# Optimization experiments

Hardware: AMD Instinct MI355X
Metric: run time of the kernel (lower is better)

## Reference

```python
import jax, jax.numpy as jnp
import numpy as np
from jax import lax

B, F_, C, H, W = 2, 1, 128, 48, 160
D = 96
MIN_DEPTH, MAX_DEPTH = 0.1, 20.0


def setup_inputs() -> dict:
    key = jax.random.key(0)
    k1, k2, k3, k4 = jax.random.split(key, 4)
    current_feats = jax.random.normal(k1, (B, C, H, W), dtype=jnp.float32)
    lookup_feats = jax.random.normal(k2, (B, F_, C, H, W), dtype=jnp.float32)
    # relative poses: identity rotation + small random translation (nonzero sum -> frame is used)
    t = np.asarray(jax.random.normal(k3, (B, F_, 3))) * 0.1
    poses = np.tile(np.eye(4, dtype=np.float32), (B, F_, 1, 1))
    poses[:, :, :3, 3] = t
    # KITTI-like intrinsics scaled to the 48x160 matching resolution
    Km = np.eye(4, dtype=np.float32)
    Km[0, 0] = 0.58 * W
    Km[1, 1] = 1.92 * H
    Km[0, 2] = 0.5 * W
    Km[1, 2] = 0.5 * H
    K = np.tile(Km, (B, 1, 1))
    invK = np.tile(np.linalg.inv(Km), (B, 1, 1))
    conv_w = jax.random.normal(k4, (C, C + D, 3, 3), dtype=jnp.float32) * 0.02
    conv_b = jnp.zeros((C,), dtype=jnp.float32)
    return {
        'current_feats': current_feats,
        'lookup_feats': lookup_feats,
        'poses': jnp.asarray(poses),
        'K': jnp.asarray(K),
        'invK': jnp.asarray(invK),
        'conv_w': conv_w,
        'conv_b': conv_b,
    }


def _plane_sweep(current_feats, lookup_feats, poses, K, invK):
    depth_bins = jnp.linspace(MIN_DEPTH, MAX_DEPTH, D).astype(jnp.float32)
    # homogeneous pixel grid [3, HW] (x, y, 1), matching BackprojectDepth
    xs, ys = jnp.meshgrid(jnp.arange(W, dtype=jnp.float32), jnp.arange(H, dtype=jnp.float32), indexing='xy')
    pix = jnp.stack([xs.ravel(), ys.ravel(), jnp.ones(H * W, jnp.float32)], 0)  # [3, HW]
    # backproject: world points per batch and depth plane -> [B, D, 4, HW]
    cam = jnp.einsum('bij,jn->bin', invK[:, :3, :3], pix)                        # [B, 3, HW]
    world = depth_bins[None, :, None, None] * cam[:, None]                       # [B, D, 3, HW]
    ones = jnp.ones((B, D, 1, H * W), jnp.float32)
    world4 = jnp.concatenate([world, ones], axis=2)                              # [B, D, 4, HW]
    # project into lookup frames (Project3D): P = (K @ T)[:3]
    P = jnp.einsum('bij,bfjk->bfik', K, poses)[:, :, :3, :]                      # [B, F, 3, 4]
    campts = jnp.einsum('bfij,bdjn->bfdin', P, world4)                           # [B, F, D, 3, HW]
    xy = campts[:, :, :, :2] / (campts[:, :, :, 2:3] + 1e-7)                     # [B, F, D, 2, HW]
    gx = xy[:, :, :, 0].reshape(B, F_, D, H, W)  # pixel x coords (align_corners=True round-trip is exact)
    gy = xy[:, :, :, 1].reshape(B, F_, D, H, W)
    # bilinear grid_sample with zeros padding
    x0 = jnp.floor(gx)
    y0 = jnp.floor(gy)
    wx = gx - x0
    wy = gy - y0
    x0i = x0.astype(jnp.int32)
    y0i = y0.astype(jnp.int32)
    x1i = x0i + 1
    y1i = y0i + 1
    feat_flat = lookup_feats.reshape(B, F_, C, H * W)
    warped = jnp.zeros((B, F_, D, C, H * W), jnp.float32)
    for xi, yi, w in ((x0i, y0i, (1 - wx) * (1 - wy)), (x1i, y0i, wx * (1 - wy)),
                      (x0i, y1i, (1 - wx) * wy), (x1i, y1i, wx * wy)):
        valid = (xi >= 0) & (xi < W) & (yi >= 0) & (yi < H)
        idx = (jnp.clip(yi, 0, H - 1) * W + jnp.clip(xi, 0, W - 1)).reshape(B, F_, D, H * W)
        vals = jnp.take_along_axis(feat_flat[:, :, None], idx[:, :, :, None], axis=4)  # [B,F,D,C,HW]
        warped = warped + vals * (w * valid.astype(jnp.float32)).reshape(B, F_, D, 1, H * W)
    warped = warped.reshape(B, F_, D, C, H, W)
    # edge mask (valid reprojections away from borders)
    edge = ((gx >= 2.0) & (gx <= W - 2) & (gy >= 2.0) & (gy <= H - 2)).astype(jnp.float32)
    interior = jnp.zeros((H, W), jnp.float32).at[2:-2, 2:-2].set(1.0)
    edge = edge * interior  # [B, F, D, H, W]
    # skip frames whose pose sums to zero
    vp = (jnp.sum(poses, axis=(2, 3)) != 0).astype(jnp.float32)                  # [B, F]
    diffs = jnp.abs(warped - current_feats[:, None, None]).mean(axis=3)          # [B, F, D, H, W]
    diffs = diffs * edge * vp[:, :, None, None, None]
    cost = jnp.sum(diffs, axis=1)                                                # [B, D, H, W]
    counts = jnp.sum((diffs > 0).astype(jnp.float32), axis=1)
    cost = cost / (counts + 1e-7)
    missing = (cost == 0).astype(jnp.float32)
    cost = cost * (1 - missing) + jnp.max(cost, axis=1, keepdims=True) * missing
    conf = (jnp.sum((cost * (1 - missing)) > 0, axis=1) == D).astype(jnp.float32)  # [B, H, W]
    viz = jnp.where(cost == 0, 100.0, cost)
    argmin = jnp.argmin(viz, axis=1)                                             # [B, H, W]
    lowest_cost = 1.0 / depth_bins[argmin]
    return cost, conf, lowest_cost


def reference(current_feats, lookup_feats, poses, K, invK, conv_w, conv_b):
    cost, conf, lowest_cost = _plane_sweep(current_feats, lookup_feats, poses, K, invK)
    cost = cost * conf[:, None]
    cat = jnp.concatenate([current_feats, cost], axis=1)                         # [B, C+D, H, W]
    out = lax.conv_general_dilated(cat, conv_w, (1, 1), 'SAME',
                                   dimension_numbers=('NCHW', 'OIHW', 'NCHW'))
    out = jax.nn.relu(out + conv_b[None, :, None, None])
    return out, lowest_cost, conf
```

## Files before the change

kernel.cpp:

```cpp
#include <hip/hip_runtime.h>
#include <hip/hip_bf16.h>

#define BB 2
#define CC 128
#define HH 48
#define WW 160
#define DD 96
#define HWp (HH*WW)
#define CIN 224
#define NKC 63
#define H2 50
#define W2 162
#define PSTR 392

typedef __bf16 bf16_t;
typedef __bf16 bf16x8 __attribute__((ext_vector_type(8)));
typedef float  f32x4  __attribute__((ext_vector_type(4)));
typedef float  f32x2  __attribute__((ext_vector_type(2)));

union ABFrag { uint4 u; bf16x8 v; };
union PackW  { bf16_t h[8]; uint4 u; };
union F4     { float4 f; f32x2 h[2]; };
union PK4    { bf16_t h[4]; uint2 u; };

#define CATP_U4 453600

__global__ __launch_bounds__(256) void k_prep(
    const float* __restrict__ look, const float* __restrict__ cw,
    float* __restrict__ lookT, bf16_t* __restrict__ wPack,
    bf16_t* __restrict__ catP) {
  int z = blockIdx.y;
  if (z < 2) {
    __shared__ float tile[CC * 65];
    int bIdx = z;
    const float* src = look + (size_t)bIdx * CC * HWp;
    int p0 = blockIdx.x * 64;
    int tid = threadIdx.x;
    int px = tid & 63, cb = tid >> 6;
    #pragma unroll
    for (int k = 0; k < 32; k++) {
      int c = k * 4 + cb;
      tile[c * 65 + px] = src[(size_t)c * HWp + p0 + px];
    }
    __syncthreads();
    int ci = tid & 127, pb = tid >> 7;
    #pragma unroll
    for (int k = 0; k < 32; k++) {
      int pp = k * 2 + pb;
      lookT[((size_t)bIdx * HWp + p0 + pp) * CC + ci] = tile[ci * 65 + pp];
    }
  } else if (z == 2) {
    for (int t = blockIdx.x * 256 + threadIdx.x; t < 8 * NKC * 64; t += 120 * 256) {
      int lane = t & 63;
      int kc = (t >> 6) % NKC;
      int nt = t / (NKC * 64);
      int co = nt * 16 + (lane & 15);
      int kbase = kc * 32 + (lane >> 4) * 8;
      PackW tmp;
      #pragma unroll
      for (int j = 0; j < 8; j++) {
        int kk = kbase + j;
        int tap = kk / 224, ci2 = kk % 224;
        int ky = tap / 3, kx = tap % 3;
        tmp.h[j] = (bf16_t)cw[(((size_t)co * 224 + ci2) * 3 + ky) * 3 + kx];
      }
      *(uint4*)(wPack + (size_t)t * 8) = tmp.u;
    }
  } else {
    uint4 zz = make_uint4(0u, 0u, 0u, 0u);
    uint4* cp = (uint4*)catP;
    for (int t = blockIdx.x * 256 + threadIdx.x; t < CATP_U4; t += 120 * 256)
      cp[t] = zz;
  }
}

__global__ __launch_bounds__(256) void k_cost(
    const float* __restrict__ cur, const float* __restrict__ lookT,
    const float* __restrict__ poses, const float* __restrict__ Kmat,
    const float* __restrict__ invK,
    bf16_t* __restrict__ catP, float* __restrict__ outLow,
    float* __restrict__ outConf) {
  __shared__ float partialL[8 * PSTR];
  __shared__ __align__(4) bf16_t fillL[8 * 96];

  int tid = threadIdx.x;
  int b = blockIdx.y;
  int wv = tid >> 6;
  int lane = tid & 63;
  int pix = lane >> 3;
  int l = lane & 7;
  int p = blockIdx.x * 8 + pix;
  int hh = p / WW, ww = p % WW;

  const float* Kb  = Kmat + b * 16;
  const float* Tb  = poses + b * 16;
  const float* iKb = invK + b * 16;
  float P[3][4];
  #pragma unroll
  for (int i = 0; i < 3; i++)
    #pragma unroll
    for (int j = 0; j < 4; j++)
      P[i][j] = Kb[i*4+0]*Tb[0*4+j] + Kb[i*4+1]*Tb[1*4+j]
              + Kb[i*4+2]*Tb[2*4+j] + Kb[i*4+3]*Tb[3*4+j];
  float psum = 0.0f;
  #pragma unroll
  for (int i = 0; i < 16; i++) psum += Tb[i];
  bool vpnz = (psum != 0.0f);

  float x = (float)ww, y = (float)hh;
  float cam0 = iKb[0]*x + iKb[1]*y + iKb[2];
  float cam1 = iKb[4]*x + iKb[5]*y + iKb[6];
  float cam2 = iKb[8]*x + iKb[9]*y + iKb[10];
  float qx = P[0][0]*cam0 + P[0][1]*cam1 + P[0][2]*cam2;
  float qy = P[1][0]*cam0 + P[1][1]*cam1 + P[1][2]*cam2;
  float qz = P[2][0]*cam0 + P[2][1]*cam1 + P[2][2]*cam2;
  float px3 = P[0][3], py3 = P[1][3], pz3 = P[2][3];
  bool interior = (hh >= 2 && hh <= HH-3 && ww >= 2 && ww <= WW-3);
  bool groupValid = interior && vpnz;

  int l4 = l * 4;
  F4 negCur[4];
  #pragma unroll
  for (int s4 = 0; s4 < 4; s4++) {
    float4 t;
    t.x = cur[((size_t)(b * CC + l4 + s4 * 32 + 0)) * HWp + p];
    t.y = cur[((size_t)(b * CC + l4 + s4 * 32 + 1)) * HWp + p];
    t.z = cur[((size_t)(b * CC + l4 + s4 * 32 + 2)) * HWp + p];
    t.w = cur[((size_t)(b * CC + l4 + s4 * 32 + 3)) * HWp + p];
    F4 tt; tt.f = t;
    negCur[s4].h[0] = -tt.h[0];
    negCur[s4].h[1] = -tt.h[1];
  }
  bf16_t* pixBase = catP + (((size_t)b * H2 + hh + 1) * W2 + (ww + 1)) * CIN;
  if (wv == 0) {
    #pragma unroll
    for (int s4 = 0; s4 < 4; s4++) {
      PK4 pk;
      pk.h[0] = (bf16_t)(-negCur[s4].f.x);
      pk.h[1] = (bf16_t)(-negCur[s4].f.y);
      pk.h[2] = (bf16_t)(-negCur[s4].f.z);
      pk.h[3] = (bf16_t)(-negCur[s4].f.w);
      *(uint2*)(pixBase + l4 + s4 * 32) = pk.u;
    }
  }

  const float* lookB = lookT + (size_t)b * HWp * CC;
  const float stepd = (20.0f - 0.1f) / 95.0f;

  int prevCell = -1;
  float x0f = 0.0f, y0f = 0.0f;
  F4 v00[4], v10[4], v01[4], v11[4];
  #pragma unroll
  for (int s4 = 0; s4 < 4; s4++) {
    v00[s4].f = make_float4(0.f,0.f,0.f,0.f);
    v10[s4].f = make_float4(0.f,0.f,0.f,0.f);
    v01[s4].f = make_float4(0.f,0.f,0.f,0.f);
    v11[s4].f = make_float4(0.f,0.f,0.f,0.f);
  }

  for (int dd = 0; dd < 24; dd++) {
    int d = wv * 24 + dd;
    float depth = 0.1f + (float)d * stepd;
    float s = 0.0f;
    if (groupValid) {
      float cxx = fmaf(depth, qx, px3);
      float cyy = fmaf(depth, qy, py3);
      float czz = fmaf(depth, qz, pz3);
      float r = __builtin_amdgcn_rcpf(czz + 1e-7f);
      float gx = cxx * r, gy = cyy * r;
      if (gx >= 2.0f && gx <= (float)(WW-2) && gy >= 2.0f && gy <= (float)(HH-2)) {
        float xf = floorf(gx), yf = floorf(gy);
        int x0 = (int)xf, y0 = (int)yf;
        int cell = y0 * WW + x0;
        if (cell != prevCell) {
          prevCell = cell; x0f = xf; y0f = yf;
          const float* bp0 = lookB + ((size_t)cell * CC + l4);
          const float* bp1 = bp0 + WW * CC;
          #pragma unroll
          for (int s4 = 0; s4 < 4; s4++) {
            v00[s4].f = *(const float4*)(bp0 + s4 * 32);
            v10[s4].f = *(const float4*)(bp0 + s4 * 32 + CC);
            v01[s4].f = *(const float4*)(bp1 + s4 * 32);
            v11[s4].f = *(const float4*)(bp1 + s4 * 32 + CC);
          }
        }
        float wx = gx - x0f, wy = gy - y0f;
        float w11v = wx * wy;
        float w10v = wx - w11v, w01v = wy - w11v;
        float w00v = 1.0f - wx - wy + w11v;
        f32x2 W00 = {w00v, w00v}, W10 = {w10v, w10v};
        f32x2 W01 = {w01v, w01v}, W11 = {w11v, w11v};
        f32x2 accA = {0.f, 0.f}, accB = {0.f, 0.f};
        #pragma unroll
        for (int s4 = 0; s4 < 4; s4++) {
          #pragma unroll
          for (int hf = 0; hf < 2; hf++) {
            f32x2 t = negCur[s4].h[hf];
            t = __builtin_elementwise_fma(W00, v00[s4].h[hf], t);
            t = __builtin_elementwise_fma(W10, v10[s4].h[hf], t);
            t = __builtin_elementwise_fma(W01, v01[s4].h[hf], t);
            t = __builtin_elementwise_fma(W11, v11[s4].h[hf], t);
            f32x2 a = __builtin_elementwise_max(t, -t);
            if (s4 & 1) accB += a; else accA += a;
          }
        }
        f32x2 accT = accA + accB;
        s = accT.x + accT.y;
      }
    }
    s += __shfl_xor(s, 1, 8);
    if ((l & 1) == 0) partialL[pix * PSTR + d * 4 + (l >> 1)] = s;
  }
  __syncthreads();

  const float kScale = 1.0f / 128.0f / (1.0f + 1e-7f);
  int pix2 = tid >> 5, g = tid & 31;
  int p2 = blockIdx.x * 8 + pix2;
  int hh2 = p2 / WW, ww2 = p2 % WW;
  float c3[3];
  float m0 = 0.0f;
  int ct = 0;
  #pragma unroll
  for (int k = 0; k < 3; k++) {
    int d = g + 32 * k;
    const float4 pp = *(const float4*)&partialL[pix2 * PSTR + d * 4];
    float c = ((pp.x + pp.y) + (pp.z + pp.w)) * kScale;
    c3[k] = c;
    m0 = fmaxf(m0, c);
    ct += (c > 0.0f) ? 1 : 0;
  }
  #pragma unroll
  for (int off = 1; off < 32; off <<= 1) {
    m0 = fmaxf(m0, __shfl_xor(m0, off, 32));
    ct += __shfl_xor(ct, off, 32);
  }
  float confF = (ct == DD) ? 1.0f : 0.0f;
  float minv = 3.4e38f;
  int mind = 0x7fffffff;
  #pragma unroll
  for (int k = 0; k < 3; k++) {
    int d = g + 32 * k;
    float c = c3[k];
    float filled = (c == 0.0f) ? m0 : c;
    float viz = (filled == 0.0f) ? 100.0f : filled;
    if (viz < minv) { minv = viz; mind = d; }
    fillL[pix2 * 96 + d] = (bf16_t)(filled * confF);
  }
  #pragma unroll
  for (int off = 1; off < 32; off <<= 1) {
    float ov = __shfl_xor(minv, off, 32);
    int   oi = __shfl_xor(mind, off, 32);
    if (ov < minv || (ov == minv && oi < mind)) { minv = ov; mind = oi; }
  }
  if (g == 0) {
    outLow[(size_t)b * HWp + p2] = 1.0f / (0.1f + (float)mind * (20.0f - 0.1f) / 95.0f);
    outConf[(size_t)b * HWp + p2] = confF;
  }
  __syncthreads();
  const unsigned* fu = (const unsigned*)fillL;
  unsigned* cu = (unsigned*)(catP + (((size_t)b * H2 + hh2 + 1) * W2 + (ww2 + 1)) * CIN + CC);
  #pragma unroll
  for (int k = 0; k < 2; k++) {
    int idx = g + 32 * k;
    if (idx < 48) cu[idx] = fu[pix2 * 48 + idx];
  }
}

__global__ __launch_bounds__(256) void k_conv(
    const bf16_t* __restrict__ catP, const bf16_t* __restrict__ wPack,
    const float* __restrict__ bias, float* __restrict__ out) {
  int wave = threadIdx.x >> 6;
  int lane = threadIdx.x & 63;
  int m16 = lane & 15, quad = lane >> 4;
  int tile = blockIdx.x * 4 + wave;
  int nt0 = blockIdx.y * 2;
  int P0 = tile * 16;
  int b = P0 / HWp;
  int rp = P0 % HWp;
  int h = rp / WW, w0 = rp % WW;

  f32x4 acc[2];
  #pragma unroll
  for (int j = 0; j < 2; j++) { f32x4 z = {0.f,0.f,0.f,0.f}; acc[j] = z; }

  #pragma unroll
  for (int tap = 0; tap < 9; tap++) {
    int dy = tap / 3 - 1, dx = tap % 3 - 1;
    const bf16_t* ap = catP
      + ((size_t)(b * H2 + h + dy + 1) * W2 + (w0 + m16 + dx + 1)) * CIN
      + quad * 8;
    #pragma unroll
    for (int sub = 0; sub < 7; sub++) {
      ABFrag a;
      a.u = *(const uint4*)(ap + sub * 32);
      int kc = tap * 7 + sub;
      #pragma unroll
      for (int j = 0; j < 2; j++) {
        ABFrag bb;
        bb.u = *(const uint4*)(wPack + (((size_t)(nt0 + j) * NKC + kc) * 64 + lane) * 8);
        acc[j] = __builtin_amdgcn_mfma_f32_16x16x32_bf16(a.v, bb.v, acc[j], 0, 0, 0);
      }
    }
  }
  #pragma unroll
  for (int j = 0; j < 2; j++) {
    int co = (nt0 + j) * 16 + m16;
    float bi = bias[co];
    #pragma unroll
    for (int r = 0; r < 4; r++) {
      int wloc = w0 + quad * 4 + r;
      float v = acc[j][r] + bi;
      v = v > 0.0f ? v : 0.0f;
      out[(((size_t)b * CC + co) * HH + h) * WW + wloc] = v;
    }
  }
}

extern "C" void kernel_launch(void* const* d_in, const int* in_sizes, int n_in,
                              void* d_out, int out_size, void* d_ws, size_t ws_size,
                              hipStream_t stream) {
  const float* cur   = (const float*)d_in[0];
  const float* look  = (const float*)d_in[1];
  const float* poses = (const float*)d_in[2];
  const float* Km    = (const float*)d_in[3];
  const float* iK    = (const float*)d_in[4];
  const float* cw    = (const float*)d_in[5];
  const float* cb    = (const float*)d_in[6];

  float* out     = (float*)d_out;
  float* outLow  = out + (size_t)BB * CC * HWp;
  float* outConf = outLow + (size_t)BB * HWp;

  char* ws = (char*)d_ws;
  float*  lookT = (float*)ws;
  bf16_t* catP  = (bf16_t*)(ws + 7864320);
  bf16_t* wPack = (bf16_t*)(ws + 7864320 + 7257600);

  k_prep<<<dim3(120, 4), 256, 0, stream>>>(look, cw, lookT, wPack, catP);
  k_cost<<<dim3(960, 2), 256, 0, stream>>>(cur, lookT, poses, Km, iK,
                                           catP, outLow, outConf);
  k_conv<<<dim3(240, 4), 256, 0, stream>>>(catP, wPack, cb, out);
}
```

Before: 153.6 us.

## Remap cost kernel so each wave sweeps all depths for four pixels

The cost kernel previously split the 96 depth planes across four waves, with each 8-lane group covering one pixel and all 128 channels. Now each 16-lane group owns one pixel and sweeps all 96 depths, with each lane holding 8 channels, and a block covers 16 pixels. Because consecutive depths of the same pixel stay in one thread, the cached bilinear corner values can be reused across more depth steps, which cuts redundant lookup loads. Register use per thread also drops. The cost is a longer serial depth loop per thread, an extra shuffle-reduction step, and half as many blocks in the grid.

```diff
diff --git a/kernel.cpp b/kernel.cpp
--- a/kernel.cpp
+++ b/kernel.cpp
@@ -11,7 +11,7 @@
 #define NKC 63
 #define H2 50
 #define W2 162
-#define PSTR 392
+#define PSTR 196
 
 typedef __bf16 bf16_t;
 typedef __bf16 bf16x8 __attribute__((ext_vector_type(8)));
@@ -80,16 +80,17 @@
     const float* __restrict__ invK,
     bf16_t* __restrict__ catP, float* __restrict__ outLow,
     float* __restrict__ outConf) {
-  __shared__ float partialL[8 * PSTR];
-  __shared__ __align__(4) bf16_t fillL[8 * 96];
+  __shared__ float partialL[16 * PSTR];
+  __shared__ __align__(4) bf16_t fillL[16 * 96];
 
   int tid = threadIdx.x;
   int b = blockIdx.y;
   int wv = tid >> 6;
   int lane = tid & 63;
-  int pix = lane >> 3;
-  int l = lane & 7;
-  int p = blockIdx.x * 8 + pix;
+  int pg = lane >> 4;
+  int l = lane & 15;
+  int pixB = wv * 4 + pg;
+  int p = blockIdx.x * 16 + pixB;
   int hh = p / WW, ww = p % WW;
 
   const float* Kb  = Kmat + b * 16;
@@ -118,30 +119,28 @@
   bool interior = (hh >= 2 && hh <= HH-3 && ww >= 2 && ww <= WW-3);
   bool groupValid = interior && vpnz;
 
-  int l4 = l * 4;
-  F4 negCur[4];
-  #pragma unroll
-  for (int s4 = 0; s4 < 4; s4++) {
+  int c0 = l * 4;
+  F4 negCur[2];
+  #pragma unroll
+  for (int s4 = 0; s4 < 2; s4++) {
     float4 t;
-    t.x = cur[((size_t)(b * CC + l4 + s4 * 32 + 0)) * HWp + p];
-    t.y = cur[((size_t)(b * CC + l4 + s4 * 32 + 1)) * HWp + p];
-    t.z = cur[((size_t)(b * CC + l4 + s4 * 32 + 2)) * HWp + p];
-    t.w = cur[((size_t)(b * CC + l4 + s4 * 32 + 3)) * HWp + p];
+    t.x = cur[((size_t)(b * CC + c0 + s4 * 64 + 0)) * HWp + p];
+    t.y = cur[((size_t)(b * CC + c0 + s4 * 64 + 1)) * HWp + p];
+    t.z = cur[((size_t)(b * CC + c0 + s4 * 64 + 2)) * HWp + p];
+    t.w = cur[((size_t)(b * CC + c0 + s4 * 64 + 3)) * HWp + p];
     F4 tt; tt.f = t;
     negCur[s4].h[0] = -tt.h[0];
     negCur[s4].h[1] = -tt.h[1];
   }
   bf16_t* pixBase = catP + (((size_t)b * H2 + hh + 1) * W2 + (ww + 1)) * CIN;
-  if (wv == 0) {
-    #pragma unroll
-    for (int s4 = 0; s4 < 4; s4++) {
-      PK4 pk;
-      pk.h[0] = (bf16_t)(-negCur[s4].f.x);
-      pk.h[1] = (bf16_t)(-negCur[s4].f.y);
-      pk.h[2] = (bf16_t)(-negCur[s4].f.z);
-      pk.h[3] = (bf16_t)(-negCur[s4].f.w);
-      *(uint2*)(pixBase + l4 + s4 * 32) = pk.u;
-    }
+  #pragma unroll
+  for (int s4 = 0; s4 < 2; s4++) {
+    PK4 pk;
+    pk.h[0] = (bf16_t)(-negCur[s4].f.x);
+    pk.h[1] = (bf16_t)(-negCur[s4].f.y);
+    pk.h[2] = (bf16_t)(-negCur[s4].f.z);
+    pk.h[3] = (bf16_t)(-negCur[s4].f.w);
+    *(uint2*)(pixBase + c0 + s4 * 64) = pk.u;
   }
 
   const float* lookB = lookT + (size_t)b * HWp * CC;
@@ -149,17 +148,16 @@
 
   int prevCell = -1;
   float x0f = 0.0f, y0f = 0.0f;
-  F4 v00[4], v10[4], v01[4], v11[4];
-  #pragma unroll
-  for (int s4 = 0; s4 < 4; s4++) {
+  F4 v00[2], v10[2], v01[2], v11[2];
+  #pragma unroll
+  for (int s4 = 0; s4 < 2; s4++) {
     v00[s4].f = make_float4(0.f,0.f,0.f,0.f);
     v10[s4].f = make_float4(0.f,0.f,0.f,0.f);
     v01[s4].f = make_float4(0.f,0.f,0.f,0.f);
     v11[s4].f = make_float4(0.f,0.f,0.f,0.f);
   }
 
-  for (int dd = 0; dd < 24; dd++) {
-    int d = wv * 24 + dd;
+  for (int d = 0; d < 96; d++) {
     float depth = 0.1f + (float)d * stepd;
     float s = 0.0f;
     if (groupValid) {
@@ -174,14 +172,14 @@
         int cell = y0 * WW + x0;
         if (cell != prevCell) {
           prevCell = cell; x0f = xf; y0f = yf;
-          const float* bp0 = lookB + ((size_t)cell * CC + l4);
+          const float* bp0 = lookB + ((size_t)cell * CC + c0);
           const float* bp1 = bp0 + WW * CC;
           #pragma unroll
-          for (int s4 = 0; s4 < 4; s4++) {
-            v00[s4].f = *(const float4*)(bp0 + s4 * 32);
-            v10[s4].f = *(const float4*)(bp0 + s4 * 32 + CC);
-            v01[s4].f = *(const float4*)(bp1 + s4 * 32);
-            v11[s4].f = *(const float4*)(bp1 + s4 * 32 + CC);
+          for (int s4 = 0; s4 < 2; s4++) {
+            v00[s4].f = *(const float4*)(bp0 + s4 * 64);
+            v10[s4].f = *(const float4*)(bp0 + s4 * 64 + CC);
+            v01[s4].f = *(const float4*)(bp1 + s4 * 64);
+            v11[s4].f = *(const float4*)(bp1 + s4 * 64 + CC);
           }
         }
         float wx = gx - x0f, wy = gy - y0f;
@@ -192,7 +190,7 @@
         f32x2 W01 = {w01v, w01v}, W11 = {w11v, w11v};
         f32x2 accA = {0.f, 0.f}, accB = {0.f, 0.f};
         #pragma unroll
-        for (int s4 = 0; s4 < 4; s4++) {
+        for (int s4 = 0; s4 < 2; s4++) {
           #pragma unroll
           for (int hf = 0; hf < 2; hf++) {
             f32x2 t = negCur[s4].h[hf];
@@ -208,48 +206,50 @@
         s = accT.x + accT.y;
       }
     }
-    s += __shfl_xor(s, 1, 8);
-    if ((l & 1) == 0) partialL[pix * PSTR + d * 4 + (l >> 1)] = s;
+    s += __shfl_xor(s, 1, 16);
+    s += __shfl_xor(s, 2, 16);
+    s += __shfl_xor(s, 4, 16);
+    if ((l & 7) == 0) partialL[pixB * PSTR + d * 2 + (l >> 3)] = s;
   }
   __syncthreads();
 
   const float kScale = 1.0f / 128.0f / (1.0f + 1e-7f);
-  int pix2 = tid >> 5, g = tid & 31;
-  int p2 = blockIdx.x * 8 + pix2;
+  int pix2 = tid >> 4, g = tid & 15;
+  int p2 = blockIdx.x * 16 + pix2;
   int hh2 = p2 / WW, ww2 = p2 % WW;
-  float c3[3];
+  float c6[6];
   float m0 = 0.0f;
   int ct = 0;
   #pragma unroll
-  for (int k = 0; k < 3; k++) {
-    int d = g + 32 * k;
-    const float4 pp = *(const float4*)&partialL[pix2 * PSTR + d * 4];
-    float c = ((pp.x + pp.y) + (pp.z + pp.w)) * kScale;
-    c3[k] = c;
+  for (int k = 0; k < 6; k++) {
+    int d = g + 16 * k;
+    const f32x2 pp = *(const f32x2*)&partialL[pix2 * PSTR + d * 2];
+    float c = (pp.x + pp.y) * kScale;
+    c6[k] = c;
     m0 = fmaxf(m0, c);
     ct += (c > 0.0f) ? 1 : 0;
   }
   #pragma unroll
-  for (int off = 1; off < 32; off <<= 1) {
-    m0 = fmaxf(m0, __shfl_xor(m0, off, 32));
-    ct += __shfl_xor(ct, off, 32);
+  for (int off = 1; off < 16; off <<= 1) {
+    m0 = fmaxf(m0, __shfl_xor(m0, off, 16));
+    ct += __shfl_xor(ct, off, 16);
   }
   float confF = (ct == DD) ? 1.0f : 0.0f;
   float minv = 3.4e38f;
   int mind = 0x7fffffff;
   #pragma unroll
-  for (int k = 0; k < 3; k++) {
-    int d = g + 32 * k;
-    float c = c3[k];
+  for (int k = 0; k < 6; k++) {
+    int d = g + 16 * k;
+    float c = c6[k];
     float filled = (c == 0.0f) ? m0 : c;
     float viz = (filled == 0.0f) ? 100.0f : filled;
     if (viz < minv) { minv = viz; mind = d; }
     fillL[pix2 * 96 + d] = (bf16_t)(filled * confF);
   }
   #pragma unroll
-  for (int off = 1; off < 32; off <<= 1) {
-    float ov = __shfl_xor(minv, off, 32);
-    int   oi = __shfl_xor(mind, off, 32);
+  for (int off = 1; off < 16; off <<= 1) {
+    float ov = __shfl_xor(minv, off, 16);
+    int   oi = __shfl_xor(mind, off, 16);
     if (ov < minv || (ov == minv && oi < mind)) { minv = ov; mind = oi; }
   }
   if (g == 0) {
@@ -260,10 +260,8 @@
   const unsigned* fu = (const unsigned*)fillL;
   unsigned* cu = (unsigned*)(catP + (((size_t)b * H2 + hh2 + 1) * W2 + (ww2 + 1)) * CIN + CC);
   #pragma unroll
-  for (int k = 0; k < 2; k++) {
-    int idx = g + 32 * k;
-    if (idx < 48) cu[idx] = fu[pix2 * 48 + idx];
-  }
+  for (int k = 0; k < 3; k++)
+    cu[g + 16 * k] = fu[pix2 * 48 + g + 16 * k];
 }
 
 __global__ __launch_bounds__(256) void k_conv(
@@ -337,7 +335,7 @@
   bf16_t* wPack = (bf16_t*)(ws + 7864320 + 7257600);
 
   k_prep<<<dim3(120, 4), 256, 0, stream>>>(look, cw, lookT, wPack, catP);
-  k_cost<<<dim3(960, 2), 256, 0, stream>>>(cur, lookT, poses, Km, iK,
+  k_cost<<<dim3(480, 2), 256, 0, stream>>>(cur, lookT, poses, Km, iK,
                                            catP, outLow, outConf);
   k_conv<<<dim3(240, 4), 256, 0, stream>>>(catP, wPack, cb, out);
 }
```

After: 173.2 us. +12.8%, slower.
